# Performance work log

Hardware: AMD Instinct MI355X
Metric: run time of the kernel (lower is better)

Reference implementation:

```python
import jax, jax.numpy as jnp
import numpy as np

SCALE = 1.0 / np.float32(64.0 ** 0.5)  # hardcoded in source, not sqrt(d)


def setup_inputs() -> dict:
    key = jax.random.key(0)
    k1, k2 = jax.random.split(key)
    B, S, D, O = 8, 2048, 768, 768
    x = jax.random.normal(k1, (B, S, D), dtype=jnp.float32)
    kernel = jax.random.normal(k2, (3, D, O), dtype=jnp.float32) * 0.02
    return {"x": x, "kernel": kernel}


def reference(x, kernel):
    # x: [B,S,D], kernel: [3,D,O]
    WQ = jnp.einsum('bsd,do->bso', x, kernel[0])
    WK = jnp.einsum('bsd,do->bso', x, kernel[1])
    WV = jnp.einsum('bsd,do->bso', x, kernel[2])
    QK = jnp.einsum('bqo,bko->bqk', WQ, WK) * SCALE  # [B,S,S]
    A = jax.nn.softmax(QK, axis=-1)
    return jnp.einsum('bqk,bko->bqo', A, WV)  # [B,S,O]
```

## Files before the change

kernel.cpp:

```cpp
#include <hip/hip_runtime.h>

typedef unsigned short u16;
typedef __attribute__((ext_vector_type(8))) short short8;
typedef __attribute__((ext_vector_type(4))) float f32x4;
typedef __attribute__((ext_vector_type(8))) unsigned short ushort8;
typedef __attribute__((ext_vector_type(4))) unsigned short ushort4v;

__device__ __forceinline__ u16 f2bf(float f) {
    unsigned int u = __float_as_uint(f);
    u += 0x7FFFu + ((u >> 16) & 1u);
    return (u16)(u >> 16);
}
__device__ __forceinline__ float bf2f(u16 h) {
    return __uint_as_float(((unsigned int)h) << 16);
}

__device__ __forceinline__ void gld_lds16(const void* g, void* l) {
    __builtin_amdgcn_global_load_lds(
        (const __attribute__((address_space(1))) unsigned int*)g,
        (__attribute__((address_space(3))) unsigned int*)l,
        16, 0, 0);
}

template <int MODE>
__global__ __launch_bounds__(256) void gemm_bt(
    const u16* __restrict__ A, const u16* __restrict__ B,
    void* __restrict__ O0, void* __restrict__ O1, void* __restrict__ O2,
    float alpha)
{
    constexpr int K   = (MODE == 2) ? 2048 : 768;
    constexpr int lda = (MODE == 2) ? 2048 : 768;
    constexpr int ldb = (MODE == 2) ? 2048 : 768;

    __shared__ u16 As[2 * 128 * 32];
    __shared__ u16 Bs[2 * 128 * 32];

    const int f = blockIdx.x;
    const int xcd = f & 7;
    const int u = f >> 3;

    int tm, bn, cn, which = 0;
    long aoff = 0, boff = 0;
    if constexpr (MODE == 0) {
        const int c = u >> 4;
        const int rl = u & 15;
        tm = (xcd * 16 + rl) * 128;
        bn = c * 128;
        which = c / 6;
        cn = (c % 6) * 128;
    } else if constexpr (MODE == 1) {
        const int p = u >> 6, t = u & 63, c = t >> 2, rl = t & 3;
        tm = (p * 4 + rl) * 128;
        bn = cn = c * 128;
        aoff = (long)xcd * 2048 * 768;
        boff = aoff;
    } else {
        const int p = u / 12, t = u % 12, c = t >> 1, rl = t & 1;
        tm = (p * 2 + rl) * 128;
        bn = cn = c * 128;
        aoff = (long)xcd * 2048 * 2048;
        boff = (long)xcd * 768 * 2048;
    }

    const u16* Ab = A + aoff;
    const u16* Bb = B + boff;

    const int tid  = threadIdx.x;
    const int lane = tid & 63;
    const int wave = tid >> 6;
    const int wr = wave >> 1;
    const int wc = wave & 1;

    f32x4 acc[4][4] = {};

    const int swz = ((lane >> 4) ^ ((lane >> 1) & 3)) * 8;
    const u16* a_base = As + (wr * 64 + (lane & 15)) * 32 + swz;
    const u16* b_base = Bs + (wc * 64 + (lane & 15)) * 32 + swz;

    const int s0 = tid, s1 = tid + 256;
    const int r0 = s0 >> 2, kc0 = (s0 & 3) ^ ((r0 >> 1) & 3);
    const int r1 = s1 >> 2, kc1 = (s1 & 3) ^ ((r1 >> 1) & 3);
    const long ar0 = (long)(tm + r0) * lda + kc0 * 8;
    const long ar1 = (long)(tm + r1) * lda + kc1 * 8;
    const long br0 = (long)(bn + r0) * ldb + kc0 * 8;
    const long br1 = (long)(bn + r1) * ldb + kc1 * 8;

#define STAGE(BUF, K0) do { \
    gld_lds16(Ab + ar0 + (K0), (void*)(As + (BUF) + s0 * 8)); \
    gld_lds16(Ab + ar1 + (K0), (void*)(As + (BUF) + s1 * 8)); \
    gld_lds16(Bb + br0 + (K0), (void*)(Bs + (BUF) + s0 * 8)); \
    gld_lds16(Bb + br1 + (K0), (void*)(Bs + (BUF) + s1 * 8)); \
} while (0)

#define COMPUTE(BUF) do { \
    short8 a[4], b[4]; \
    _Pragma("unroll") \
    for (int i = 0; i < 4; ++i) a[i] = *(const short8*)(a_base + (BUF) + i * 16 * 32); \
    _Pragma("unroll") \
    for (int j = 0; j < 4; ++j) b[j] = *(const short8*)(b_base + (BUF) + j * 16 * 32); \
    _Pragma("unroll") \
    for (int i = 0; i < 4; ++i) \
    _Pragma("unroll") \
        for (int j = 0; j < 4; ++j) \
            acc[i][j] = __builtin_amdgcn_mfma_f32_16x16x32_bf16( \
                a[i], b[j], acc[i][j], 0, 0, 0); \
} while (0)

    STAGE(0, 0);
    __syncthreads();

#pragma unroll 1
    for (int k0 = 0; k0 < K; k0 += 64) {
        STAGE(4096, k0 + 32);
        COMPUTE(0);
        __syncthreads();
        if (k0 + 64 < K) STAGE(0, k0 + 64);
        COMPUTE(4096);
        __syncthreads();
    }

#undef STAGE
#undef COMPUTE

#pragma unroll
    for (int i = 0; i < 4; ++i) {
        const int row0 = tm + wr * 64 + i * 16 + ((lane >> 4) << 2);
#pragma unroll
        for (int j = 0; j < 4; ++j) {
            const int col = cn + wc * 64 + j * 16 + (lane & 15);
#pragma unroll
            for (int r = 0; r < 4; ++r) {
                const int row = row0 + r;
                const float val = acc[i][j][r] * alpha;
                if constexpr (MODE == 0) {
                    if (which == 0)
                        ((u16*)O0)[(long)row * 768 + col] = f2bf(val);
                    else if (which == 1)
                        ((u16*)O1)[(long)row * 768 + col] = f2bf(val);
                    else
                        ((u16*)O2)[((long)(row >> 11) * 768 + col) * 2048 + (row & 2047)] = f2bf(val);
                } else if constexpr (MODE == 1) {
                    ((u16*)O0)[(long)xcd * 2048 * 2048 + (long)row * 2048 + col] = f2bf(val);
                } else {
                    ((float*)O0)[(long)xcd * 2048 * 768 + (long)row * 768 + col] = val;
                }
            }
        }
    }
}

__global__ __launch_bounds__(256) void cvt_x_kernel(
    const float4* __restrict__ x, ushort4v* __restrict__ out, int n4)
{
    int i = blockIdx.x * 256 + threadIdx.x;
    if (i < n4) {
        float4 f = x[i];
        ushort4v o;
        o.x = f2bf(f.x); o.y = f2bf(f.y); o.z = f2bf(f.z); o.w = f2bf(f.w);
        out[i] = o;
    }
}

__global__ __launch_bounds__(256) void cvt_w_kernel(
    const float* __restrict__ w, u16* __restrict__ wt)
{
    int i = blockIdx.x * 256 + threadIdx.x;
    int d = i % 768;
    int o = (i / 768) % 768;
    int m = i / (768 * 768);
    wt[i] = f2bf(w[((long)m * 768 + d) * 768 + o]);
}

__global__ __launch_bounds__(256) void softmax_kernel(u16* __restrict__ S)
{
    const long row = blockIdx.x;
    u16* p = S + row * 2048;
    const int t = threadIdx.x;
    const int lane = t & 63;
    const int wave = t >> 6;
    __shared__ float red[8];

    ushort8 raw = *(const ushort8*)(p + t * 8);
    float v[8];
    float m = -1e30f;
#pragma unroll
    for (int i = 0; i < 8; ++i) { v[i] = bf2f(raw[i]); m = fmaxf(m, v[i]); }
#pragma unroll
    for (int off = 1; off < 64; off <<= 1) m = fmaxf(m, __shfl_xor(m, off, 64));
    if (lane == 0) red[wave] = m;
    __syncthreads();
    m = fmaxf(fmaxf(red[0], red[1]), fmaxf(red[2], red[3]));

    float s = 0.f;
#pragma unroll
    for (int i = 0; i < 8; ++i) { v[i] = __expf(v[i] - m); s += v[i]; }
#pragma unroll
    for (int off = 1; off < 64; off <<= 1) s += __shfl_xor(s, off, 64);
    if (lane == 0) red[4 + wave] = s;
    __syncthreads();
    s = (red[4] + red[5]) + (red[6] + red[7]);

    const float inv = 1.0f / s;
    ushort8 out;
#pragma unroll
    for (int i = 0; i < 8; ++i) out[i] = f2bf(v[i] * inv);
    *(ushort8*)(p + t * 8) = out;
}

extern "C" void kernel_launch(void* const* d_in, const int* in_sizes, int n_in,
                              void* d_out, int out_size, void* d_ws, size_t ws_size,
                              hipStream_t stream)
{
    const float* x  = (const float*)d_in[0];
    const float* wk = (const float*)d_in[1];
    float* out = (float*)d_out;

    char* ws = (char*)d_ws;
    u16* xbf = (u16*)(ws);
    u16* wt  = (u16*)(ws + 25165824);
    u16* qbf = (u16*)(ws + 28704768);
    u16* kbf = (u16*)(ws + 53870592);
    u16* vt  = (u16*)(ws + 79036416);
    u16* S   = (u16*)(ws + 104202240);

    cvt_x_kernel<<<dim3(12288), dim3(256), 0, stream>>>(
        (const float4*)x, (ushort4v*)xbf, 3145728);
    cvt_w_kernel<<<dim3(6912), dim3(256), 0, stream>>>(wk, wt);

    gemm_bt<0><<<dim3(2304), dim3(256), 0, stream>>>(
        xbf, wt, qbf, kbf, vt, 1.0f);

    gemm_bt<1><<<dim3(2048), dim3(256), 0, stream>>>(
        qbf, kbf, S, nullptr, nullptr, 0.125f);

    softmax_kernel<<<dim3(16384), dim3(256), 0, stream>>>(S);

    gemm_bt<2><<<dim3(768), dim3(256), 0, stream>>>(
        S, vt, out, nullptr, nullptr, 1.0f);
}
```

Before: 364.3 us.

## Stage GEMM tiles through registers with single-buffered XOR-swizzled 64-wide LDS

Replaces the direct global-to-LDS async loads and double-buffered 32-wide K tiles with register-staged global loads. The next 64-wide K tile is prefetched into registers while the current tile is computed, then written to a single XOR-swizzled LDS buffer. Launch bounds now request 3 blocks per SM. The aim is to hide global latency behind compute and to cut barriers per K step, at the cost of extra VGPRs for staging and an extra barrier around the LDS write.

```diff
diff --git a/kernel.cpp b/kernel.cpp
--- a/kernel.cpp
+++ b/kernel.cpp
@@ -15,15 +15,8 @@
     return __uint_as_float(((unsigned int)h) << 16);
 }
 
-__device__ __forceinline__ void gld_lds16(const void* g, void* l) {
-    __builtin_amdgcn_global_load_lds(
-        (const __attribute__((address_space(1))) unsigned int*)g,
-        (__attribute__((address_space(3))) unsigned int*)l,
-        16, 0, 0);
-}
-
 template <int MODE>
-__global__ __launch_bounds__(256) void gemm_bt(
+__global__ __launch_bounds__(256, 3) void gemm_bt(
     const u16* __restrict__ A, const u16* __restrict__ B,
     void* __restrict__ O0, void* __restrict__ O1, void* __restrict__ O2,
     float alpha)
@@ -32,8 +25,8 @@
     constexpr int lda = (MODE == 2) ? 2048 : 768;
     constexpr int ldb = (MODE == 2) ? 2048 : 768;
 
-    __shared__ u16 As[2 * 128 * 32];
-    __shared__ u16 Bs[2 * 128 * 32];
+    __shared__ __align__(16) u16 As[128 * 64];
+    __shared__ __align__(16) u16 Bs[128 * 64];
 
     const int f = blockIdx.x;
     const int xcd = f & 7;
@@ -73,31 +66,43 @@
 
     f32x4 acc[4][4] = {};
 
-    const int swz = ((lane >> 4) ^ ((lane >> 1) & 3)) * 8;
-    const u16* a_base = As + (wr * 64 + (lane & 15)) * 32 + swz;
-    const u16* b_base = Bs + (wc * 64 + (lane & 15)) * 32 + swz;
-
-    const int s0 = tid, s1 = tid + 256;
-    const int r0 = s0 >> 2, kc0 = (s0 & 3) ^ ((r0 >> 1) & 3);
-    const int r1 = s1 >> 2, kc1 = (s1 & 3) ^ ((r1 >> 1) & 3);
-    const long ar0 = (long)(tm + r0) * lda + kc0 * 8;
-    const long ar1 = (long)(tm + r1) * lda + kc1 * 8;
-    const long br0 = (long)(bn + r0) * ldb + kc0 * 8;
-    const long br1 = (long)(bn + r1) * ldb + kc1 * 8;
-
-#define STAGE(BUF, K0) do { \
-    gld_lds16(Ab + ar0 + (K0), (void*)(As + (BUF) + s0 * 8)); \
-    gld_lds16(Ab + ar1 + (K0), (void*)(As + (BUF) + s1 * 8)); \
-    gld_lds16(Bb + br0 + (K0), (void*)(Bs + (BUF) + s0 * 8)); \
-    gld_lds16(Bb + br1 + (K0), (void*)(Bs + (BUF) + s1 * 8)); \
+    const int srow = tid >> 3;
+    const int sg   = tid & 7;
+    const int dcol = (sg ^ (srow & 7)) * 8;
+    const u16* Agp = Ab + (long)(tm + srow) * lda + sg * 8;
+    const u16* Bgp = Bb + (long)(bn + srow) * ldb + sg * 8;
+    u16* Adst = As + srow * 64 + dcol;
+    u16* Bdst = Bs + srow * 64 + dcol;
+
+    uint4 ra[4], rb[4];
+
+#define LOADR(K0) do { _Pragma("unroll") \
+    for (int p = 0; p < 4; ++p) { \
+        ra[p] = *(const uint4*)(Agp + (K0) + (long)p * 32 * lda); \
+        rb[p] = *(const uint4*)(Bgp + (K0) + (long)p * 32 * ldb); } \
 } while (0)
 
-#define COMPUTE(BUF) do { \
+#define DSWR() do { _Pragma("unroll") \
+    for (int p = 0; p < 4; ++p) { \
+        *(uint4*)(Adst + p * 32 * 64) = ra[p]; \
+        *(uint4*)(Bdst + p * 32 * 64) = rb[p]; } \
+} while (0)
+
+    const int rrow = lane & 15;
+    const int lx   = lane & 7;
+    const int g0 = ((lane >> 4)    ) ^ lx;
+    const int g1 = ((lane >> 4) | 4) ^ lx;
+    const u16* a0 = As + (wr * 64 + rrow) * 64 + g0 * 8;
+    const u16* a1 = As + (wr * 64 + rrow) * 64 + g1 * 8;
+    const u16* b0 = Bs + (wc * 64 + rrow) * 64 + g0 * 8;
+    const u16* b1 = Bs + (wc * 64 + rrow) * 64 + g1 * 8;
+
+#define HALF(AP, BP) do { \
     short8 a[4], b[4]; \
     _Pragma("unroll") \
-    for (int i = 0; i < 4; ++i) a[i] = *(const short8*)(a_base + (BUF) + i * 16 * 32); \
-    _Pragma("unroll") \
-    for (int j = 0; j < 4; ++j) b[j] = *(const short8*)(b_base + (BUF) + j * 16 * 32); \
+    for (int i = 0; i < 4; ++i) a[i] = *(const short8*)((AP) + i * 16 * 64); \
+    _Pragma("unroll") \
+    for (int j = 0; j < 4; ++j) b[j] = *(const short8*)((BP) + j * 16 * 64); \
     _Pragma("unroll") \
     for (int i = 0; i < 4; ++i) \
     _Pragma("unroll") \
@@ -106,21 +111,26 @@
                 a[i], b[j], acc[i][j], 0, 0, 0); \
 } while (0)
 
-    STAGE(0, 0);
+    LOADR(0);
+    DSWR();
     __syncthreads();
 
 #pragma unroll 1
     for (int k0 = 0; k0 < K; k0 += 64) {
-        STAGE(4096, k0 + 32);
-        COMPUTE(0);
+        const bool more = (k0 + 64 < K);
+        if (more) LOADR(k0 + 64);
+        HALF(a0, b0);
+        HALF(a1, b1);
         __syncthreads();
-        if (k0 + 64 < K) STAGE(0, k0 + 64);
-        COMPUTE(4096);
-        __syncthreads();
-    }
-
-#undef STAGE
-#undef COMPUTE
+        if (more) {
+            DSWR();
+            __syncthreads();
+        }
+    }
+
+#undef HALF
+#undef DSWR
+#undef LOADR
 
 #pragma unroll
     for (int i = 0; i < 4; ++i) {
```

New measurement: 867.8 us. +138.2%, slower.

## Widen GEMM tiles to 128x256 and drop LDS double buffering

Applied to the files above, without the earlier changes.

All three GEMM launches move from 128x128 to 128x256 output tiles, so each wave computes a 64x128 sub-tile with 32 accumulators. This halves the block count and raises arithmetic intensity per loaded A fragment. The K loop is now single-buffered with 32-wide steps and two barriers per iteration, removing the prefetch overlap that the double-buffered loop provided. Launch bounds request 2 blocks per CU to limit register use. The bigger accumulator set risks spilling, and MODE 2 now launches only 384 blocks, which could underfill the GPU.

```diff
diff --git a/kernel.cpp b/kernel.cpp
--- a/kernel.cpp
+++ b/kernel.cpp
@@ -23,7 +23,7 @@
 }
 
 template <int MODE>
-__global__ __launch_bounds__(256) void gemm_bt(
+__global__ __launch_bounds__(256, 2) void gemm_bt(
     const u16* __restrict__ A, const u16* __restrict__ B,
     void* __restrict__ O0, void* __restrict__ O1, void* __restrict__ O2,
     float alpha)
@@ -32,8 +32,8 @@
     constexpr int lda = (MODE == 2) ? 2048 : 768;
     constexpr int ldb = (MODE == 2) ? 2048 : 768;
 
-    __shared__ u16 As[2 * 128 * 32];
-    __shared__ u16 Bs[2 * 128 * 32];
+    __shared__ u16 As[128 * 32];
+    __shared__ u16 Bs[256 * 32];
 
     const int f = blockIdx.x;
     const int xcd = f & 7;
@@ -45,19 +45,19 @@
         const int c = u >> 4;
         const int rl = u & 15;
         tm = (xcd * 16 + rl) * 128;
-        bn = c * 128;
-        which = c / 6;
-        cn = (c % 6) * 128;
+        bn = c * 256;
+        which = c / 3;
+        cn = (c % 3) * 256;
     } else if constexpr (MODE == 1) {
-        const int p = u >> 6, t = u & 63, c = t >> 2, rl = t & 3;
+        const int p = u >> 5, t = u & 31, c = t >> 2, rl = t & 3;
         tm = (p * 4 + rl) * 128;
-        bn = cn = c * 128;
+        bn = cn = c * 256;
         aoff = (long)xcd * 2048 * 768;
         boff = aoff;
     } else {
-        const int p = u / 12, t = u % 12, c = t >> 1, rl = t & 1;
+        const int p = u / 6, t = u % 6, c = t >> 1, rl = t & 1;
         tm = (p * 2 + rl) * 128;
-        bn = cn = c * 128;
+        bn = cn = c * 256;
         aoff = (long)xcd * 2048 * 2048;
         boff = (long)xcd * 768 * 2048;
     }
@@ -71,52 +71,51 @@
     const int wr = wave >> 1;
     const int wc = wave & 1;
 
-    f32x4 acc[4][4] = {};
+    f32x4 acc[4][8] = {};
 
     const int swz = ((lane >> 4) ^ ((lane >> 1) & 3)) * 8;
     const u16* a_base = As + (wr * 64 + (lane & 15)) * 32 + swz;
-    const u16* b_base = Bs + (wc * 64 + (lane & 15)) * 32 + swz;
-
-    const int s0 = tid, s1 = tid + 256;
-    const int r0 = s0 >> 2, kc0 = (s0 & 3) ^ ((r0 >> 1) & 3);
-    const int r1 = s1 >> 2, kc1 = (s1 & 3) ^ ((r1 >> 1) & 3);
-    const long ar0 = (long)(tm + r0) * lda + kc0 * 8;
-    const long ar1 = (long)(tm + r1) * lda + kc1 * 8;
-    const long br0 = (long)(bn + r0) * ldb + kc0 * 8;
-    const long br1 = (long)(bn + r1) * ldb + kc1 * 8;
-
-#define STAGE(BUF, K0) do { \
-    gld_lds16(Ab + ar0 + (K0), (void*)(As + (BUF) + s0 * 8)); \
-    gld_lds16(Ab + ar1 + (K0), (void*)(As + (BUF) + s1 * 8)); \
-    gld_lds16(Bb + br0 + (K0), (void*)(Bs + (BUF) + s0 * 8)); \
-    gld_lds16(Bb + br1 + (K0), (void*)(Bs + (BUF) + s1 * 8)); \
+    const u16* b_base = Bs + (wc * 128 + (lane & 15)) * 32 + swz;
+
+    const int sA0 = tid, sA1 = tid + 256;
+    const int ra0 = sA0 >> 2, ka0 = (sA0 & 3) ^ ((ra0 >> 1) & 3);
+    const int ra1 = sA1 >> 2, ka1 = (sA1 & 3) ^ ((ra1 >> 1) & 3);
+    const long arow0 = (long)(tm + ra0) * lda + ka0 * 8;
+    const long arow1 = (long)(tm + ra1) * lda + ka1 * 8;
+    const int rb = tid >> 2, kb = (tid & 3) ^ ((rb >> 1) & 3);
+    long brow[4];
+#pragma unroll
+    for (int q = 0; q < 4; ++q)
+        brow[q] = (long)(bn + rb + 64 * q) * ldb + kb * 8;
+
+#define STAGE(K0) do { \
+    gld_lds16(Ab + arow0 + (K0), (void*)(As + sA0 * 8)); \
+    gld_lds16(Ab + arow1 + (K0), (void*)(As + sA1 * 8)); \
+    _Pragma("unroll") \
+    for (int q = 0; q < 4; ++q) \
+        gld_lds16(Bb + brow[q] + (K0), (void*)(Bs + tid * 8 + q * 2048)); \
 } while (0)
 
-#define COMPUTE(BUF) do { \
-    short8 a[4], b[4]; \
+#define COMPUTE() do { \
+    short8 a[4]; \
     _Pragma("unroll") \
-    for (int i = 0; i < 4; ++i) a[i] = *(const short8*)(a_base + (BUF) + i * 16 * 32); \
+    for (int i = 0; i < 4; ++i) a[i] = *(const short8*)(a_base + i * 16 * 32); \
     _Pragma("unroll") \
-    for (int j = 0; j < 4; ++j) b[j] = *(const short8*)(b_base + (BUF) + j * 16 * 32); \
-    _Pragma("unroll") \
-    for (int i = 0; i < 4; ++i) \
-    _Pragma("unroll") \
-        for (int j = 0; j < 4; ++j) \
+    for (int j = 0; j < 8; ++j) { \
+        const short8 bj = *(const short8*)(b_base + j * 16 * 32); \
+        _Pragma("unroll") \
+        for (int i = 0; i < 4; ++i) \
             acc[i][j] = __builtin_amdgcn_mfma_f32_16x16x32_bf16( \
-                a[i], b[j], acc[i][j], 0, 0, 0); \
+                a[i], bj, acc[i][j], 0, 0, 0); \
+    } \
 } while (0)
 
-    STAGE(0, 0);
-    __syncthreads();
-
 #pragma unroll 1
-    for (int k0 = 0; k0 < K; k0 += 64) {
-        STAGE(4096, k0 + 32);
-        COMPUTE(0);
+    for (int k0 = 0; k0 < K; k0 += 32) {
         __syncthreads();
-        if (k0 + 64 < K) STAGE(0, k0 + 64);
-        COMPUTE(4096);
+        STAGE(k0);
         __syncthreads();
+        COMPUTE();
     }
 
 #undef STAGE
@@ -126,8 +125,8 @@
     for (int i = 0; i < 4; ++i) {
         const int row0 = tm + wr * 64 + i * 16 + ((lane >> 4) << 2);
 #pragma unroll
-        for (int j = 0; j < 4; ++j) {
-            const int col = cn + wc * 64 + j * 16 + (lane & 15);
+        for (int j = 0; j < 8; ++j) {
+            const int col = cn + wc * 128 + j * 16 + (lane & 15);
 #pragma unroll
             for (int r = 0; r < 4; ++r) {
                 const int row = row0 + r;
@@ -227,14 +226,14 @@
         (const float4*)x, (ushort4v*)xbf, 3145728);
     cvt_w_kernel<<<dim3(6912), dim3(256), 0, stream>>>(wk, wt);
 
-    gemm_bt<0><<<dim3(2304), dim3(256), 0, stream>>>(
+    gemm_bt<0><<<dim3(1152), dim3(256), 0, stream>>>(
         xbf, wt, qbf, kbf, vt, 1.0f);
 
-    gemm_bt<1><<<dim3(2048), dim3(256), 0, stream>>>(
+    gemm_bt<1><<<dim3(1024), dim3(256), 0, stream>>>(
         qbf, kbf, S, nullptr, nullptr, 0.125f);
 
     softmax_kernel<<<dim3(16384), dim3(256), 0, stream>>>(S);
 
-    gemm_bt<2><<<dim3(768), dim3(256), 0, stream>>>(
+    gemm_bt<2><<<dim3(384), dim3(256), 0, stream>>>(
         S, vt, out, nullptr, nullptr, 1.0f);
 }
```

Result: slower. 373.3 us (+2.5%).

## Use single-buffered 64-wide K tiles with new XOR swizzle in GEMM

Applied to the files above, without the earlier changes.

Replaces the double-buffered 32-wide K staging with a single 128x64 LDS tile per operand, loaded in one stage per iteration with an 8-way XOR swizzle. Each iteration does two MFMA half-passes over the tile. This halves barrier count per K and uses wider rows, but removes overlap between global-to-LDS loads and compute, since loads now sit between two barriers before compute.

```diff
diff --git a/kernel.cpp b/kernel.cpp
--- a/kernel.cpp
+++ b/kernel.cpp
@@ -32,8 +32,8 @@
     constexpr int lda = (MODE == 2) ? 2048 : 768;
     constexpr int ldb = (MODE == 2) ? 2048 : 768;
 
-    __shared__ u16 As[2 * 128 * 32];
-    __shared__ u16 Bs[2 * 128 * 32];
+    __shared__ u16 As[128 * 64];
+    __shared__ u16 Bs[128 * 64];
 
     const int f = blockIdx.x;
     const int xcd = f & 7;
@@ -73,31 +73,34 @@
 
     f32x4 acc[4][4] = {};
 
-    const int swz = ((lane >> 4) ^ ((lane >> 1) & 3)) * 8;
-    const u16* a_base = As + (wr * 64 + (lane & 15)) * 32 + swz;
-    const u16* b_base = Bs + (wc * 64 + (lane & 15)) * 32 + swz;
-
-    const int s0 = tid, s1 = tid + 256;
-    const int r0 = s0 >> 2, kc0 = (s0 & 3) ^ ((r0 >> 1) & 3);
-    const int r1 = s1 >> 2, kc1 = (s1 & 3) ^ ((r1 >> 1) & 3);
-    const long ar0 = (long)(tm + r0) * lda + kc0 * 8;
-    const long ar1 = (long)(tm + r1) * lda + kc1 * 8;
-    const long br0 = (long)(bn + r0) * ldb + kc0 * 8;
-    const long br1 = (long)(bn + r1) * ldb + kc1 * 8;
-
-#define STAGE(BUF, K0) do { \
-    gld_lds16(Ab + ar0 + (K0), (void*)(As + (BUF) + s0 * 8)); \
-    gld_lds16(Ab + ar1 + (K0), (void*)(As + (BUF) + s1 * 8)); \
-    gld_lds16(Bb + br0 + (K0), (void*)(Bs + (BUF) + s0 * 8)); \
-    gld_lds16(Bb + br1 + (K0), (void*)(Bs + (BUF) + s1 * 8)); \
+    const int sr = tid >> 3;
+    const int gs = tid & 7;
+    const int g  = gs ^ (sr & 7);
+    const long arow = (long)(tm + sr) * lda + g * 8;
+    const long brow = (long)(bn + sr) * ldb + g * 8;
+
+#define STAGE(K0) do { _Pragma("unroll") \
+    for (int k = 0; k < 4; ++k) { \
+        gld_lds16(Ab + arow + (long)k * 32 * lda + (K0), (void*)(As + (tid + 256 * k) * 8)); \
+        gld_lds16(Bb + brow + (long)k * 32 * ldb + (K0), (void*)(Bs + (tid + 256 * k) * 8)); \
+    } \
 } while (0)
 
-#define COMPUTE(BUF) do { \
+    const int rr = lane & 15;
+    const int lx = lane & 7;
+    const int q0 = ((lane >> 4)    ) ^ lx;
+    const int q1 = ((lane >> 4) | 4) ^ lx;
+    const u16* a0 = As + (wr * 64 + rr) * 64 + q0 * 8;
+    const u16* a1 = As + (wr * 64 + rr) * 64 + q1 * 8;
+    const u16* b0 = Bs + (wc * 64 + rr) * 64 + q0 * 8;
+    const u16* b1 = Bs + (wc * 64 + rr) * 64 + q1 * 8;
+
+#define HALF(AP, BP) do { \
     short8 a[4], b[4]; \
     _Pragma("unroll") \
-    for (int i = 0; i < 4; ++i) a[i] = *(const short8*)(a_base + (BUF) + i * 16 * 32); \
-    _Pragma("unroll") \
-    for (int j = 0; j < 4; ++j) b[j] = *(const short8*)(b_base + (BUF) + j * 16 * 32); \
+    for (int i = 0; i < 4; ++i) a[i] = *(const short8*)((AP) + i * 16 * 64); \
+    _Pragma("unroll") \
+    for (int j = 0; j < 4; ++j) b[j] = *(const short8*)((BP) + j * 16 * 64); \
     _Pragma("unroll") \
     for (int i = 0; i < 4; ++i) \
     _Pragma("unroll") \
@@ -106,21 +109,17 @@
                 a[i], b[j], acc[i][j], 0, 0, 0); \
 } while (0)
 
-    STAGE(0, 0);
-    __syncthreads();
-
 #pragma unroll 1
     for (int k0 = 0; k0 < K; k0 += 64) {
-        STAGE(4096, k0 + 32);
-        COMPUTE(0);
         __syncthreads();
-        if (k0 + 64 < K) STAGE(0, k0 + 64);
-        COMPUTE(4096);
+        STAGE(k0);
         __syncthreads();
-    }
-
+        HALF(a0, b0);
+        HALF(a1, b1);
+    }
+
+#undef HALF
 #undef STAGE
-#undef COMPUTE
 
 #pragma unroll
     for (int i = 0; i < 4; ++i) {
```

After: 334.7 us. 8.1% less time.
